# Kernel optimization log

Hardware: AMD Instinct MI355X
Metric: run time of the kernel (lower is better)

## Reference

```python
import jax, jax.numpy as jnp
import numpy as np

B = 16384
D = 4096  # d_mlp == d_hidden in this module
K = 64


def setup_inputs() -> dict:
    key = jax.random.key(0)
    k1, k2, k3, k4 = jax.random.split(key, 4)
    x = jax.random.normal(k1, (B, D), dtype=jnp.float32)
    ema_frequency_counter = jax.random.uniform(k2, (D,), dtype=jnp.float32)
    W_enc = jax.random.normal(k3, (D, D), dtype=jnp.float32)
    # W_dec initialized like the module: randn, then scaled by 0.1/(norm+2*eps-ish);
    # the exact init scaling: norm over dim=1, norm += eps(=1), then *= 0.1/(norm+eps)
    W_dec_raw = jax.random.normal(k4, (D, D), dtype=jnp.float32)
    eps = 1.0
    norm = jnp.linalg.norm(W_dec_raw, axis=1, keepdims=True) + eps
    W_dec = W_dec_raw * (0.1 / (norm + eps))
    pre_bias = jnp.zeros((D,), dtype=jnp.float32)
    latent_bias = jnp.zeros((D,), dtype=jnp.float32)
    return {
        'x': x,
        'ema_frequency_counter': ema_frequency_counter,
        'W_enc': W_enc,
        'W_dec': W_dec,
        'pre_bias': pre_bias,
        'latent_bias': latent_bias,
        'k': K,
    }


def topk_activation(acts, k):
    # torch.topk -> ReLU on values -> scatter back into zeros
    vals, idx = jax.lax.top_k(acts, k)          # [B, k]
    vals = jax.nn.relu(vals)
    rows = jnp.arange(acts.shape[0])[:, None]   # [B, 1]
    return jnp.zeros_like(acts).at[rows, idx].set(vals)


def reference(x, ema_frequency_counter, W_enc, W_dec, pre_bias, latent_bias, k):
    # method='reconstruct' path of TopKAutoEncoder.forward
    x_center = x - pre_bias                     # [B, D]
    acts = x_center @ W_enc + latent_bias       # [B, D]
    acts_top_k = topk_activation(acts, k)       # sparse (k nonzeros/row)
    x_reconstruct = acts_top_k @ W_dec + pre_bias
    return x_reconstruct
```

## Files before the change

kernel.cpp:

```cpp
#include <hip/hip_runtime.h>
#include <hip/hip_bf16.h>
#include <stdint.h>


typedef _Float16 half8 __attribute__((ext_vector_type(8)));
typedef float f32x4 __attribute__((ext_vector_type(4)));
typedef unsigned short ushort8 __attribute__((ext_vector_type(8)));

#define B_ROWS 16384
#define D_DIM  4096
#define TOPK   64
#define MARGIN 0.25f
#define NTILES (D_DIM / 32)

__device__ __forceinline__ void gload_lds16(const void* g, void* l) {
  __builtin_amdgcn_global_load_lds(
      (const __attribute__((address_space(1))) unsigned int*)g,
      (__attribute__((address_space(3))) unsigned int*)l, 16, 0, 0);
}

__device__ __forceinline__ unsigned short f2bf(float f) {
  unsigned u = __float_as_uint(f);
  unsigned r = (u + 0x7fffu + ((u >> 16) & 1u)) >> 16;
  return (unsigned short)r;
}


__global__ __launch_bounds__(256) void conv_x(
    const float* __restrict__ x, const float* __restrict__ pre_bias,
    _Float16* __restrict__ Xh) {
  size_t g = ((size_t)blockIdx.x * 256 + threadIdx.x) * 8;
  int col = (int)(g & (D_DIM - 1));
  float4 a = *(const float4*)(x + g);
  float4 b = *(const float4*)(x + g + 4);
  float4 p = *(const float4*)(pre_bias + col);
  float4 q = *(const float4*)(pre_bias + col + 4);
  half8 h;
  h[0] = (_Float16)(a.x - p.x); h[1] = (_Float16)(a.y - p.y);
  h[2] = (_Float16)(a.z - p.z); h[3] = (_Float16)(a.w - p.w);
  h[4] = (_Float16)(b.x - q.x); h[5] = (_Float16)(b.y - q.y);
  h[6] = (_Float16)(b.z - q.z); h[7] = (_Float16)(b.w - q.w);
  *(half8*)(Xh + g) = h;
}

__global__ __launch_bounds__(256) void transp_w(
    const float* __restrict__ W, _Float16* __restrict__ WhT,
    float* __restrict__ WT) {
  __shared__ float tile[64][65];
  int bx = blockIdx.x, by = blockIdx.y;
  int tx = threadIdx.x & 63, ty4 = threadIdx.x >> 6;
  #pragma unroll 4
  for (int i = 0; i < 16; ++i) {
    int r = ty4 * 16 + i;
    tile[r][tx] = W[(size_t)(by * 64 + r) * D_DIM + bx * 64 + tx];
  }
  __syncthreads();
  #pragma unroll 4
  for (int i = 0; i < 16; ++i) {
    int r = ty4 * 16 + i;
    float v = tile[tx][r];
    size_t o = (size_t)(bx * 64 + r) * D_DIM + by * 64 + tx;
    WT[o] = v;
    WhT[o] = (_Float16)v;
  }
}

__global__ __launch_bounds__(256) void conv_wd(
    const float* __restrict__ W, unsigned short* __restrict__ o) {
  size_t g = ((size_t)blockIdx.x * 256 + threadIdx.x) * 8;
  float4 a = *(const float4*)(W + g);
  float4 b = *(const float4*)(W + g + 4);
  ushort8 v;
  v[0] = f2bf(a.x); v[1] = f2bf(a.y); v[2] = f2bf(a.z); v[3] = f2bf(a.w);
  v[4] = f2bf(b.x); v[5] = f2bf(b.y); v[6] = f2bf(b.z); v[7] = f2bf(b.w);
  *(ushort8*)(o + g) = v;
}


#define TILE_BODY(T, VMSTR)                                                    \
  do {                                                                         \
    asm volatile("s_waitcnt " VMSTR ::: "memory");                             \
    __builtin_amdgcn_s_barrier();                                              \
    asm volatile("" ::: "memory");                                             \
    const int tt3 = (T) + 3;                                                   \
    if (tt3 < NTILES) {                                                        \
      const int bo = (tt3 & 3) * 8192;                                         \
      const int kk = tt3 * 32;                                                 \
      gload_lds16(aSrc + kk, AsB + bo + dstL);                                 \
      gload_lds16(bSrc + kk, BsB + bo + dstL);                                 \
    }                                                                          \
    {                                                                          \
      const int ab = ((T) & 3) * 8192;                                         \
      half8 bf[4], af[4];                                                      \
      _Pragma("unroll") for (int nj = 0; nj < 4; ++nj)                         \
          bf[nj] = *(const half8*)(BsB + ab + bBase + nj * 512);               \
      _Pragma("unroll") for (int mi = 0; mi < 4; ++mi)                         \
          af[mi] = *(const half8*)(AsB + ab + aBase + mi * 512);               \
      __builtin_amdgcn_s_setprio(1);                                           \
      _Pragma("unroll") for (int mi = 0; mi < 4; ++mi)                         \
          _Pragma("unroll") for (int nj = 0; nj < 4; ++nj)                     \
          acc[mi][nj] = __builtin_amdgcn_mfma_f32_16x16x32_f16(                \
              af[mi], bf[nj], acc[mi][nj], 0, 0, 0);                           \
      __builtin_amdgcn_s_setprio(0);                                           \
    }                                                                          \
  } while (0)

__global__ __launch_bounds__(1024, 4) void gemm_f16(
    const _Float16* __restrict__ A, const _Float16* __restrict__ Bt,
    const float* __restrict__ latent_bias, float* __restrict__ C) {
  extern __shared__ _Float16 ldsbuf[];
  _Float16* AsB = ldsbuf;
  _Float16* BsB = ldsbuf + 4 * 8192;

  const int tid = threadIdx.x;
  const int lane = tid & 63, wave = tid >> 6;
  const int wm = wave >> 2, wn = wave & 3;

  int bid = blockIdx.x;
  int swz = (bid & 7) * (1024 >> 3) + (bid >> 3);
  const int bmBase = (swz >> 4) * 256;
  const int bnBase = (swz & 15) * 256;

  const int s = tid ^ ((tid >> 3) & 3);
  const _Float16* aSrc = A + (size_t)(bmBase + (s >> 2)) * D_DIM + (s & 3) * 8;
  const _Float16* bSrc = Bt + (size_t)(bnBase + (s >> 2)) * D_DIM + (s & 3) * 8;
  const int dstL = tid * 8;

  const int fr = lane & 15, c4 = lane >> 4;
  const int swzc = (c4 ^ ((fr >> 1) & 3)) * 8;
  const int aBase = (wm * 64 + fr) * 32 + swzc;
  const int bBase = (wn * 64 + fr) * 32 + swzc;

  f32x4 acc[4][4];
  #pragma unroll
  for (int i = 0; i < 4; ++i)
    #pragma unroll
    for (int j = 0; j < 4; ++j) acc[i][j] = f32x4{0.f, 0.f, 0.f, 0.f};

  #pragma unroll
  for (int tt = 0; tt < 3; ++tt) {
    const int bo = tt * 8192, kk = tt * 32;
    gload_lds16(aSrc + kk, AsB + bo + dstL);
    gload_lds16(bSrc + kk, BsB + bo + dstL);
  }

  for (int t = 0; t < NTILES - 2; ++t) TILE_BODY(t, "vmcnt(4)");
  TILE_BODY(NTILES - 2, "vmcnt(2)");
  TILE_BODY(NTILES - 1, "vmcnt(0)");

  const int crow0 = bmBase + wm * 64 + c4 * 4;
  const int ccol0 = bnBase + wn * 64 + fr;
  #pragma unroll
  for (int mi = 0; mi < 4; ++mi)
    #pragma unroll
    for (int nj = 0; nj < 4; ++nj) {
      int col = ccol0 + nj * 16;
      float lb = latent_bias[col];
      #pragma unroll
      for (int r = 0; r < 4; ++r)
        C[(size_t)(crow0 + mi * 16 + r) * D_DIM + col] = acc[mi][nj][r] + lb;
    }
}


__global__ __launch_bounds__(256) void topk_classify(
    const float* __restrict__ acts, float* __restrict__ vals,
    int* __restrict__ idxs, int* __restrict__ ambIdx,
    int* __restrict__ rowMeta) {
  const int row = blockIdx.x;
  const int tid = threadIdx.x;
  const int lane = tid & 63, wave = tid >> 6;
  __shared__ int hist[4096];
  __shared__ int sred[8];
  const float* arow = acts + (size_t)row * D_DIM;
  float fv[16];
  #pragma unroll
  for (int i = 0; i < 4; ++i) {
    float4 a = *(const float4*)(arow + i * 1024 + tid * 4);
    fv[4 * i + 0] = a.x; fv[4 * i + 1] = a.y;
    fv[4 * i + 2] = a.z; fv[4 * i + 3] = a.w;
  }
  #pragma unroll
  for (int i = 0; i < 16; ++i) hist[tid * 16 + i] = 0;
  __syncthreads();
  #pragma unroll
  for (int e = 0; e < 16; ++e) {
    int b = (int)((fv[e] + 512.0f) * 4.0f);
    b = b < 0 ? 0 : (b > 4095 ? 4095 : b);
    atomicAdd(&hist[b], 1);
  }
  __syncthreads();
  int loc[16];
  int s = 0;
  #pragma unroll
  for (int i = 15; i >= 0; --i) { s += hist[tid * 16 + i]; loc[i] = s; }
  int x = s;
  #pragma unroll
  for (int off = 1; off < 64; off <<= 1) {
    int y = __shfl_down(x, off);
    if (lane + off < 64) x += y;
  }
  if (lane == 0) sred[wave] = x;
  __syncthreads();
  int after = 0;
  for (int w = wave + 1; w < 4; ++w) after += sred[w];
  const int sufAfter = (x - s) + after;
  int cand = -1;
  #pragma unroll
  for (int i = 0; i < 16; ++i)
    if (loc[i] + sufAfter >= TOPK) cand = tid * 16 + i;
  #pragma unroll
  for (int off = 32; off; off >>= 1) {
    int y = __shfl_down(cand, off);
    cand = y > cand ? y : cand;
  }
  if (lane == 0) sred[4 + wave] = cand;
  __syncthreads();
  int b0 = sred[4] > sred[5] ? sred[4] : sred[5];
  int b1 = sred[6] > sred[7] ? sred[6] : sred[7];
  const int bstar = b0 > b1 ? b0 : b1;
  const float Tlo = (bstar == 0) ? -1e30f : (bstar * 0.25f - 512.0f);
  const float Thi = (bstar >= 4095) ? 1e30f : ((bstar + 1) * 0.25f - 512.0f);
  const float vhi = Thi + MARGIN;
  const float vlo = Tlo - MARGIN;
  int mC = 0, aC = 0;
  #pragma unroll
  for (int i = 0; i < 16; ++i) {
    float v = fv[i];
    if (v > vhi) ++mC;
    else if (v >= vlo) ++aC;
  }
  int xs = mC | (aC << 16);
  #pragma unroll
  for (int off = 1; off < 64; off <<= 1) {
    int y = __shfl_up(xs, off);
    if (lane >= off) xs += y;
  }
  if (lane == 63) sred[wave] = xs;
  __syncthreads();
  int base = 0;
  for (int w = 0; w < 4; ++w)
    if (w < wave) base += sred[w];
  int tot = sred[0] + sred[1] + sred[2] + sred[3];
  int incl = base + xs;
  int mp = (incl & 0xffff) - mC;
  int ap = (incl >> 16) - aC;
  int mTot = tot & 0xffff, aTot = tot >> 16;
  const int need = TOPK - mTot;
  const bool fast = (aTot == need);
  #pragma unroll
  for (int e = 0; e < 16; ++e) {
    float v = fv[e];
    int d = (e >> 2) * 1024 + tid * 4 + (e & 3);
    if (v > vhi) {
      vals[(size_t)row * TOPK + mp] = fmaxf(v, 0.0f);
      idxs[(size_t)row * TOPK + mp] = d;
      ++mp;
    } else if (v >= vlo) {
      if (fast) {
        vals[(size_t)row * TOPK + mTot + ap] = fmaxf(v, 0.0f);
        idxs[(size_t)row * TOPK + mTot + ap] = d;
      } else if (ap < 128) {
        ambIdx[(size_t)row * 128 + ap] = d;
      }
      ++ap;
    }
  }
  if (tid == 0) {
    rowMeta[row * 2 + 0] = mTot;
    rowMeta[row * 2 + 1] = (fast || need <= 0) ? 0 : ((aTot > 128) ? 128 : aTot);
  }
}


__global__ __launch_bounds__(256) void rescue(
    const float* __restrict__ x, const float* __restrict__ WT,
    const float* __restrict__ pre_bias, const float* __restrict__ latent_bias,
    const float* __restrict__ acts, const int* __restrict__ ambIdx,
    const int* __restrict__ rowMeta, float* __restrict__ vals,
    int* __restrict__ idxs) {
  const int row = blockIdx.x;
  const int m = rowMeta[row * 2 + 0];
  const int s = rowMeta[row * 2 + 1];
  const int need = TOPK - m;
  const int tid = threadIdx.x;
  if (need <= 0 || s <= 0) return;
  if (s == need) {
    if (tid < s) {
      int d = ambIdx[(size_t)row * 128 + tid];
      float v = acts[(size_t)row * D_DIM + d];
      vals[(size_t)row * TOPK + m + tid] = fmaxf(v, 0.0f);
      idxs[(size_t)row * TOPK + m + tid] = d;
    }
    return;
  }
  __shared__ double exv[128];
  const int lane = tid & 63, wave = tid >> 6;
  const float* xr = x + (size_t)row * D_DIM;
  for (int c = wave; c < s; c += 4) {
    int d = ambIdx[(size_t)row * 128 + c];
    const float* wrow = WT + (size_t)d * D_DIM;
    double acc = 0.0;
    #pragma unroll 4
    for (int t = 0; t < 16; ++t) {
      int k0 = t * 256 + lane * 4;
      float4 xv = *(const float4*)(xr + k0);
      float4 pv = *(const float4*)(pre_bias + k0);
      float4 wv = *(const float4*)(wrow + k0);
      acc = fma((double)xv.x - (double)pv.x, (double)wv.x, acc);
      acc = fma((double)xv.y - (double)pv.y, (double)wv.y, acc);
      acc = fma((double)xv.z - (double)pv.z, (double)wv.z, acc);
      acc = fma((double)xv.w - (double)pv.w, (double)wv.w, acc);
    }
    #pragma unroll
    for (int off = 32; off; off >>= 1) acc += __shfl_down(acc, off);
    if (lane == 0) exv[c] = acc + (double)latent_bias[d];
  }
  __syncthreads();
  if (tid == 0) {
    for (int t = 0; t < need; ++t) {
      double best = -1.0e300; int besti = 1 << 30; int bestc = -1;
      for (int c = 0; c < s; ++c) {
        double v = exv[c];
        int d = ambIdx[(size_t)row * 128 + c];
        if (v > best || (v == best && d < besti)) {
          best = v; besti = d; bestc = c;
        }
      }
      vals[(size_t)row * TOPK + m + t] = fmaxf((float)best, 0.0f);
      idxs[(size_t)row * TOPK + m + t] = besti;
      exv[bestc] = -1.0e300;
    }
  }
}


__global__ __launch_bounds__(256) void reconstruct(
    const unsigned short* __restrict__ Wd, const float* __restrict__ vals,
    const int* __restrict__ idxs, const float* __restrict__ pre_bias,
    float* __restrict__ out) {
  const int bid = blockIdx.x;
  const int cb = bid & 7, rowblk = bid >> 3;
  const int tid = threadIdx.x, lane = tid & 63, wave = tid >> 6;
  const int row = rowblk * 4 + wave;
  const int col0 = cb * 512 + lane * 8;
  __shared__ float sval[256];
  __shared__ int sidx[256];
  sval[tid] = vals[(size_t)(rowblk * 4 + (tid >> 6)) * TOPK + (tid & 63)];
  sidx[tid] = idxs[(size_t)(rowblk * 4 + (tid >> 6)) * TOPK + (tid & 63)];
  __syncthreads();
  float acc[8];
  float4 p0 = *(const float4*)(pre_bias + col0);
  float4 p1 = *(const float4*)(pre_bias + col0 + 4);
  acc[0] = p0.x; acc[1] = p0.y; acc[2] = p0.z; acc[3] = p0.w;
  acc[4] = p1.x; acc[5] = p1.y; acc[6] = p1.z; acc[7] = p1.w;
  #pragma unroll 4
  for (int k = 0; k < TOPK; ++k) {
    float v = sval[wave * 64 + k];
    int d = sidx[wave * 64 + k];
    ushort8 w = *(const ushort8*)(Wd + (size_t)d * D_DIM + col0);
    #pragma unroll
    for (int j = 0; j < 8; ++j)
      acc[j] = fmaf(v, __uint_as_float(((unsigned)w[j]) << 16), acc[j]);
  }
  float4 o0 = {acc[0], acc[1], acc[2], acc[3]};
  float4 o1 = {acc[4], acc[5], acc[6], acc[7]};
  *(float4*)(out + (size_t)row * D_DIM + col0) = o0;
  *(float4*)(out + (size_t)row * D_DIM + col0 + 4) = o1;
}


extern "C" void kernel_launch(void* const* d_in, const int* in_sizes, int n_in,
                              void* d_out, int out_size, void* d_ws,
                              size_t ws_size, hipStream_t stream) {
  const float* x           = (const float*)d_in[0];
  const float* W_enc       = (const float*)d_in[2];
  const float* W_dec       = (const float*)d_in[3];
  const float* pre_bias    = (const float*)d_in[4];
  const float* latent_bias = (const float*)d_in[5];
  float* out = (float*)d_out;
  char* ws = (char*)d_ws;
  size_t off = 0;
  auto alloc = [&](size_t bytes) {
    size_t o = off;
    off = (off + bytes + 255) & ~(size_t)255;
    return o;
  };
  _Float16* Xh        = (_Float16*)(ws + alloc((size_t)B_ROWS * D_DIM * 2));
  _Float16* WhT       = (_Float16*)(ws + alloc((size_t)D_DIM * D_DIM * 2));
  float* WT           = (float*)(ws + alloc((size_t)D_DIM * D_DIM * 4));
  unsigned short* Wd  = (unsigned short*)(ws + alloc((size_t)D_DIM * D_DIM * 2));
  float* vals         = (float*)(ws + alloc((size_t)B_ROWS * TOPK * 4));
  int* idxs           = (int*)(ws + alloc((size_t)B_ROWS * TOPK * 4));
  int* ambIdx         = (int*)(ws + alloc((size_t)B_ROWS * 128 * 4));
  int* rowMeta        = (int*)(ws + alloc((size_t)B_ROWS * 2 * 4));
  (void)ws_size; (void)in_sizes; (void)n_in; (void)out_size;

  (void)hipFuncSetAttribute((const void*)gemm_f16,
                            hipFuncAttributeMaxDynamicSharedMemorySize,
                            131072);

  conv_x<<<(B_ROWS * D_DIM / 8) / 256, 256, 0, stream>>>(x, pre_bias, Xh);
  transp_w<<<dim3(D_DIM / 64, D_DIM / 64), 256, 0, stream>>>(W_enc, WhT, WT);
  conv_wd<<<((size_t)D_DIM * D_DIM / 8) / 256, 256, 0, stream>>>(W_dec, Wd);
  gemm_f16<<<(B_ROWS / 256) * (D_DIM / 256), 1024, 131072, stream>>>(
      Xh, WhT, latent_bias, out);
  topk_classify<<<B_ROWS, 256, 0, stream>>>(out, vals, idxs, ambIdx, rowMeta);
  rescue<<<B_ROWS, 256, 0, stream>>>(x, WT, pre_bias, latent_bias, out,
                                     ambIdx, rowMeta, vals, idxs);
  reconstruct<<<(B_ROWS / 4) * 8, 256, 0, stream>>>(Wd, vals, idxs, pre_bias,
                                                    out);
}
```

Baseline: 1.155 ms.

## Fuse top-k classify and rescue kernels with two-level 256-bin histogram

Merges the classification and rescue kernels into a single per-row kernel, so the ambiguous candidate indices stay in shared memory and the global ambIdx/rowMeta buffers and one kernel launch go away. The single 4096-bin histogram is replaced by a coarse 256-bin pass followed by a fine 256-bin pass over the selected coarse bin. This cuts LDS zeroing and the per-thread scan work. In exchange it adds extra barriers and a second atomic pass. The fused kernel also carries the rescue code's shared arrays and registers, which may reduce occupancy.

```diff
diff --git a/kernel.cpp b/kernel.cpp
--- a/kernel.cpp
+++ b/kernel.cpp
@@ -163,15 +163,19 @@
 }
 
 
-__global__ __launch_bounds__(256) void topk_classify(
-    const float* __restrict__ acts, float* __restrict__ vals,
-    int* __restrict__ idxs, int* __restrict__ ambIdx,
-    int* __restrict__ rowMeta) {
+__global__ __launch_bounds__(256) void topk_full(
+    const float* __restrict__ acts, const float* __restrict__ x,
+    const float* __restrict__ WT, const float* __restrict__ pre_bias,
+    const float* __restrict__ latent_bias, float* __restrict__ vals,
+    int* __restrict__ idxs) {
   const int row = blockIdx.x;
   const int tid = threadIdx.x;
   const int lane = tid & 63, wave = tid >> 6;
-  __shared__ int hist[4096];
+  __shared__ int hist[256];
+  __shared__ int suf[256];
   __shared__ int sred[8];
+  __shared__ int ambL[128];
+  __shared__ double exv[128];
   const float* arow = acts + (size_t)row * D_DIM;
   float fv[16];
   #pragma unroll
@@ -180,47 +184,92 @@
     fv[4 * i + 0] = a.x; fv[4 * i + 1] = a.y;
     fv[4 * i + 2] = a.z; fv[4 * i + 3] = a.w;
   }
-  #pragma unroll
-  for (int i = 0; i < 16; ++i) hist[tid * 16 + i] = 0;
+  hist[tid] = 0;
   __syncthreads();
   #pragma unroll
   for (int e = 0; e < 16; ++e) {
-    int b = (int)((fv[e] + 512.0f) * 4.0f);
-    b = b < 0 ? 0 : (b > 4095 ? 4095 : b);
+    int b = (int)((fv[e] + 512.0f) * 0.25f);
+    b = b < 0 ? 0 : (b > 255 ? 255 : b);
     atomicAdd(&hist[b], 1);
   }
   __syncthreads();
-  int loc[16];
-  int s = 0;
-  #pragma unroll
-  for (int i = 15; i >= 0; --i) { s += hist[tid * 16 + i]; loc[i] = s; }
-  int x = s;
+  int c = hist[tid];
+  int sfx = c;
   #pragma unroll
   for (int off = 1; off < 64; off <<= 1) {
-    int y = __shfl_down(x, off);
-    if (lane + off < 64) x += y;
-  }
-  if (lane == 0) sred[wave] = x;
-  __syncthreads();
-  int after = 0;
-  for (int w = wave + 1; w < 4; ++w) after += sred[w];
-  const int sufAfter = (x - s) + after;
-  int cand = -1;
-  #pragma unroll
-  for (int i = 0; i < 16; ++i)
-    if (loc[i] + sufAfter >= TOPK) cand = tid * 16 + i;
+    int y = __shfl_down(sfx, off);
+    if (lane + off < 64) sfx += y;
+  }
+  if (lane == 0) sred[wave] = sfx;
+  __syncthreads();
+  {
+    int after = 0;
+    for (int w = wave + 1; w < 4; ++w) after += sred[w];
+    sfx += after;
+  }
+  suf[tid] = sfx;
+  int cnd = (sfx >= TOPK) ? tid : -1;
   #pragma unroll
   for (int off = 32; off; off >>= 1) {
-    int y = __shfl_down(cand, off);
-    cand = y > cand ? y : cand;
-  }
-  if (lane == 0) sred[4 + wave] = cand;
-  __syncthreads();
-  int b0 = sred[4] > sred[5] ? sred[4] : sred[5];
-  int b1 = sred[6] > sred[7] ? sred[6] : sred[7];
-  const int bstar = b0 > b1 ? b0 : b1;
-  const float Tlo = (bstar == 0) ? -1e30f : (bstar * 0.25f - 512.0f);
-  const float Thi = (bstar >= 4095) ? 1e30f : ((bstar + 1) * 0.25f - 512.0f);
+    int y = __shfl_down(cnd, off);
+    cnd = y > cnd ? y : cnd;
+  }
+  if (lane == 0) sred[4 + wave] = cnd;
+  __syncthreads();
+  int cb;
+  {
+    int m0 = sred[4] > sred[5] ? sred[4] : sred[5];
+    int m1 = sred[6] > sred[7] ? sred[6] : sred[7];
+    cb = m0 > m1 ? m0 : m1;
+  }
+  const int S_above = (cb < 255) ? suf[cb + 1] : 0;
+  const int rrank = TOPK - S_above;
+  const float Clo = cb * 4.0f - 512.0f;
+  __syncthreads();
+  hist[tid] = 0;
+  __syncthreads();
+  #pragma unroll
+  for (int e = 0; e < 16; ++e) {
+    int bc = (int)((fv[e] + 512.0f) * 0.25f);
+    bc = bc < 0 ? 0 : (bc > 255 ? 255 : bc);
+    if (bc == cb) {
+      int fb = (int)((fv[e] - Clo) * 64.0f);
+      fb = fb < 0 ? 0 : (fb > 255 ? 255 : fb);
+      atomicAdd(&hist[fb], 1);
+    }
+  }
+  __syncthreads();
+  int cf = hist[tid];
+  int sfx2 = cf;
+  #pragma unroll
+  for (int off = 1; off < 64; off <<= 1) {
+    int y = __shfl_down(sfx2, off);
+    if (lane + off < 64) sfx2 += y;
+  }
+  if (lane == 0) sred[wave] = sfx2;
+  __syncthreads();
+  {
+    int after = 0;
+    for (int w = wave + 1; w < 4; ++w) after += sred[w];
+    sfx2 += after;
+  }
+  int cnd2 = (sfx2 >= rrank) ? tid : -1;
+  #pragma unroll
+  for (int off = 32; off; off >>= 1) {
+    int y = __shfl_down(cnd2, off);
+    cnd2 = y > cnd2 ? y : cnd2;
+  }
+  if (lane == 0) sred[4 + wave] = cnd2;
+  __syncthreads();
+  int fb;
+  {
+    int m0 = sred[4] > sred[5] ? sred[4] : sred[5];
+    int m1 = sred[6] > sred[7] ? sred[6] : sred[7];
+    fb = m0 > m1 ? m0 : m1;
+  }
+  const float Tlo = (cb == 0 && fb == 0) ? -1e30f : (Clo + fb * 0.015625f);
+  const float Thi =
+      (cb == 255 && fb == 255) ? 1e30f : (Clo + (fb + 1) * 0.015625f);
   const float vhi = Thi + MARGIN;
   const float vlo = Tlo - MARGIN;
   int mC = 0, aC = 0;
@@ -236,6 +285,7 @@
     int y = __shfl_up(xs, off);
     if (lane >= off) xs += y;
   }
+  __syncthreads();
   if (lane == 63) sred[wave] = xs;
   __syncthreads();
   int base = 0;
@@ -261,44 +311,17 @@
         vals[(size_t)row * TOPK + mTot + ap] = fmaxf(v, 0.0f);
         idxs[(size_t)row * TOPK + mTot + ap] = d;
       } else if (ap < 128) {
-        ambIdx[(size_t)row * 128 + ap] = d;
+        ambL[ap] = d;
       }
       ++ap;
     }
   }
-  if (tid == 0) {
-    rowMeta[row * 2 + 0] = mTot;
-    rowMeta[row * 2 + 1] = (fast || need <= 0) ? 0 : ((aTot > 128) ? 128 : aTot);
-  }
-}
-
-
-__global__ __launch_bounds__(256) void rescue(
-    const float* __restrict__ x, const float* __restrict__ WT,
-    const float* __restrict__ pre_bias, const float* __restrict__ latent_bias,
-    const float* __restrict__ acts, const int* __restrict__ ambIdx,
-    const int* __restrict__ rowMeta, float* __restrict__ vals,
-    int* __restrict__ idxs) {
-  const int row = blockIdx.x;
-  const int m = rowMeta[row * 2 + 0];
-  const int s = rowMeta[row * 2 + 1];
-  const int need = TOPK - m;
-  const int tid = threadIdx.x;
-  if (need <= 0 || s <= 0) return;
-  if (s == need) {
-    if (tid < s) {
-      int d = ambIdx[(size_t)row * 128 + tid];
-      float v = acts[(size_t)row * D_DIM + d];
-      vals[(size_t)row * TOPK + m + tid] = fmaxf(v, 0.0f);
-      idxs[(size_t)row * TOPK + m + tid] = d;
-    }
-    return;
-  }
-  __shared__ double exv[128];
-  const int lane = tid & 63, wave = tid >> 6;
+  if (fast) return;
+  __syncthreads();
+  const int sN = aTot > 128 ? 128 : aTot;
   const float* xr = x + (size_t)row * D_DIM;
-  for (int c = wave; c < s; c += 4) {
-    int d = ambIdx[(size_t)row * 128 + c];
+  for (int cc = wave; cc < sN; cc += 4) {
+    int d = ambL[cc];
     const float* wrow = WT + (size_t)d * D_DIM;
     double acc = 0.0;
     #pragma unroll 4
@@ -314,21 +337,21 @@
     }
     #pragma unroll
     for (int off = 32; off; off >>= 1) acc += __shfl_down(acc, off);
-    if (lane == 0) exv[c] = acc + (double)latent_bias[d];
+    if (lane == 0) exv[cc] = acc + (double)latent_bias[d];
   }
   __syncthreads();
   if (tid == 0) {
     for (int t = 0; t < need; ++t) {
       double best = -1.0e300; int besti = 1 << 30; int bestc = -1;
-      for (int c = 0; c < s; ++c) {
-        double v = exv[c];
-        int d = ambIdx[(size_t)row * 128 + c];
+      for (int cc = 0; cc < sN; ++cc) {
+        double v = exv[cc];
+        int d = ambL[cc];
         if (v > best || (v == best && d < besti)) {
-          best = v; besti = d; bestc = c;
+          best = v; besti = d; bestc = cc;
         }
       }
-      vals[(size_t)row * TOPK + m + t] = fmaxf((float)best, 0.0f);
-      idxs[(size_t)row * TOPK + m + t] = besti;
+      vals[(size_t)row * TOPK + mTot + t] = fmaxf((float)best, 0.0f);
+      idxs[(size_t)row * TOPK + mTot + t] = besti;
       exv[bestc] = -1.0e300;
     }
   }
@@ -392,8 +415,6 @@
   unsigned short* Wd  = (unsigned short*)(ws + alloc((size_t)D_DIM * D_DIM * 2));
   float* vals         = (float*)(ws + alloc((size_t)B_ROWS * TOPK * 4));
   int* idxs           = (int*)(ws + alloc((size_t)B_ROWS * TOPK * 4));
-  int* ambIdx         = (int*)(ws + alloc((size_t)B_ROWS * 128 * 4));
-  int* rowMeta        = (int*)(ws + alloc((size_t)B_ROWS * 2 * 4));
   (void)ws_size; (void)in_sizes; (void)n_in; (void)out_size;
 
   (void)hipFuncSetAttribute((const void*)gemm_f16,
@@ -405,9 +426,8 @@
   conv_wd<<<((size_t)D_DIM * D_DIM / 8) / 256, 256, 0, stream>>>(W_dec, Wd);
   gemm_f16<<<(B_ROWS / 256) * (D_DIM / 256), 1024, 131072, stream>>>(
       Xh, WhT, latent_bias, out);
-  topk_classify<<<B_ROWS, 256, 0, stream>>>(out, vals, idxs, ambIdx, rowMeta);
-  rescue<<<B_ROWS, 256, 0, stream>>>(x, WT, pre_bias, latent_bias, out,
-                                     ambIdx, rowMeta, vals, idxs);
+  topk_full<<<B_ROWS, 256, 0, stream>>>(out, x, WT, pre_bias, latent_bias,
+                                        vals, idxs);
   reconstruct<<<(B_ROWS / 4) * 8, 256, 0, stream>>>(Wd, vals, idxs, pre_bias,
                                                     out);
 }
```

Result: no change. 1.148 ms (-0.6%).
